# Kernel tuning notes

Measured on AMD Instinct MI355X. Metric: run time of the kernel, lower is better.

Reference implementation:

```python
import jax, jax.numpy as jnp
import numpy as np

SLOPE = 25.0   # fast_sigmoid surrogate slope (affects backward only)
THRESH = 1.0   # snntorch Leaky default threshold

@jax.custom_vjp
def spike(x):
    # Heaviside forward, fast-sigmoid surrogate backward
    return (x > 0).astype(x.dtype)

def _spike_fwd(x):
    return spike(x), x

def _spike_bwd(x, g):
    return (g / (SLOPE * jnp.abs(x) + 1.0) ** 2,)

spike.defvjp(_spike_fwd, _spike_bwd)


def setup_inputs() -> dict:
    key = jax.random.key(0)
    ks = jax.random.split(key, 16)
    B, T, F = 512, 1024, 64
    SNN, H, HOR = 128, 128, 24
    s = 0.05
    inp = {
        "x": jax.random.normal(ks[0], (B, T, F), jnp.float32),
        "proj_w": jax.random.normal(ks[1], (SNN, F), jnp.float32) * s,
        "proj_b": jnp.zeros((SNN,), jnp.float32),
        "beta1": jnp.full((SNN,), 0.9, jnp.float32),
        "beta2": jnp.full((SNN,), 0.9, jnp.float32),
        "gru_w_ih": jax.random.normal(ks[2], (3 * H, F + SNN), jnp.float32) * s,
        "gru_w_hh": jax.random.normal(ks[3], (3 * H, H), jnp.float32) * s,
        "gru_b_ih": jnp.zeros((3 * H,), jnp.float32),
        "gru_b_hh": jnp.zeros((3 * H,), jnp.float32),
        "attn_w1": jax.random.normal(ks[4], (H // 2, H), jnp.float32) * s,
        "attn_b1": jnp.zeros((H // 2,), jnp.float32),
        "attn_w2": jax.random.normal(ks[5], (1, H // 2), jnp.float32) * s,
        "attn_b2": jnp.zeros((1,), jnp.float32),
        "head_w": jax.random.normal(ks[6], (HOR, H), jnp.float32) * s,
        "head_b": jnp.zeros((HOR,), jnp.float32),
    }
    return inp


def reference(x, proj_w, proj_b, beta1, beta2,
              gru_w_ih, gru_w_hh, gru_b_ih, gru_b_hh,
              attn_w1, attn_b1, attn_w2, attn_b2, head_w, head_b):
    b1 = jnp.clip(beta1, 0.0, 0.99)
    b2 = jnp.clip(beta2, 0.0, 0.99)

    delta = x[:, 1:, :] - x[:, :-1, :]   # (B, T-1, F)
    raw = x[:, 1:, :]
    h_s = delta @ proj_w.T + proj_b      # (B, T-1, SNN)

    B = x.shape[0]
    SNN = proj_w.shape[0]

    # snntorch Leaky (subtract reset, reset from previous step's spike):
    # mem_t = beta*mem_{t-1} + in_t - spk_{t-1}*thr ; spk_t = H(mem_t - thr)
    def snn_step(carry, inp_t):
        m1, s1, m2, s2 = carry
        m1 = b1 * m1 + inp_t - s1 * THRESH
        s1n = spike(m1 - THRESH)
        m2 = b2 * m2 + s1n - s2 * THRESH
        s2n = spike(m2 - THRESH)
        return (m1, s1n, m2, s2n), m2

    z = jnp.zeros((B, SNN), x.dtype)
    _, mem_rec = jax.lax.scan(snn_step, (z, z, z, z), jnp.swapaxes(h_s, 0, 1))
    h_snn = jnp.swapaxes(mem_rec, 0, 1)             # (B, T-1, SNN)

    h_comb = jnp.concatenate([raw, h_snn], axis=-1)  # (B, T-1, F+SNN)

    # GRU (PyTorch gate layout: r, z, n)
    H = gru_w_hh.shape[1]
    x_proj = h_comb @ gru_w_ih.T + gru_b_ih          # (B, T-1, 3H)

    def gru_step(h, xp):
        gh = h @ gru_w_hh.T + gru_b_hh
        xr, xz, xn = jnp.split(xp, 3, axis=-1)
        hr, hz, hn = jnp.split(gh, 3, axis=-1)
        r = jax.nn.sigmoid(xr + hr)
        zg = jax.nn.sigmoid(xz + hz)
        n = jnp.tanh(xn + r * hn)
        h_new = (1.0 - zg) * n + zg * h
        return h_new, h_new

    h0 = jnp.zeros((B, H), x.dtype)
    _, gru_seq = jax.lax.scan(gru_step, h0, jnp.swapaxes(x_proj, 0, 1))
    gru_out = jnp.swapaxes(gru_seq, 0, 1)            # (B, T-1, H)

    # Temporal attention over time (dim=1)
    scores = jax.nn.relu(gru_out @ attn_w1.T + attn_b1) @ attn_w2.T + attn_b2  # (B, T-1, 1)
    w = jax.nn.softmax(scores, axis=1)
    h_ann = (w * gru_out).sum(axis=1)                # (B, H)

    return h_ann @ head_w.T + head_b                 # (B, horizon)
```

## Files before the change

kernel.cpp:

```cpp
#include <hip/hip_runtime.h>

typedef unsigned short u16;
typedef __attribute__((ext_vector_type(8))) short short8;
typedef __attribute__((ext_vector_type(4))) float f32x4;

__device__ __forceinline__ u16 f2bf(float f) {
  union { float f; unsigned u; } v; v.f = f;
  unsigned r = v.u + 0x7fffu + ((v.u >> 16) & 1u);
  return (u16)(r >> 16);
}
__device__ __forceinline__ u16 truncbf(float f) {
  union { float f; unsigned u; } v; v.f = f;
  return (u16)(v.u >> 16);
}
__device__ __forceinline__ float bf2f(u16 h) {
  union { unsigned u; float f; } v; v.u = ((unsigned)h) << 16;
  return v.f;
}
__device__ __forceinline__ void gll16(const void* g, void* l) {
  __builtin_amdgcn_global_load_lds((const __attribute__((address_space(1))) unsigned*)g,
                                   (__attribute__((address_space(3))) unsigned*)l, 16, 0, 0);
}
__device__ __forceinline__ void bar_lds() {
  asm volatile("s_waitcnt lgkmcnt(0)" ::: "memory");
  __builtin_amdgcn_s_barrier();
  asm volatile("" ::: "memory");
}

#define BATCH 512
#define TS 1023
#define NF 64
#define NS 128
#define NH 128
#define NG 384
#define NC 192
#define TCH 341

__global__ void k_prep(const float* __restrict__ wih, const float* __restrict__ w1,
                       u16* __restrict__ wihb, u16* __restrict__ w1b) {
  int i = blockIdx.x * 256 + threadIdx.x;
  if (i < NG * NC) wihb[i] = f2bf(wih[i]);
  if (i < 64 * NH) w1b[i] = f2bf(w1[i]);
}

__global__ __launch_bounds__(256, 2) void k_front(const float* __restrict__ x,
                                                  const float* __restrict__ pw,
                                                  const float* __restrict__ pb,
                                                  const float* __restrict__ beta1,
                                                  const float* __restrict__ beta2,
                                                  u16* __restrict__ hcomb) {
  __shared__ float hst[64 * 138];
  const int tid = threadIdx.x, lane = tid & 63, w = tid >> 6;
  const int m16 = lane & 15, quad = lane >> 4;
  const int b = blockIdx.x;
  const float* xb = x + (long)b * 65536;

  const int tm = (w >> 1) * 32, nn = (w & 1) * 64;

  short8 bh[2][4], bl[2][4];
  #pragma unroll
  for (int kc = 0; kc < 2; ++kc)
    #pragma unroll
    for (int ni = 0; ni < 4; ++ni) {
      const float* src = pw + (nn + ni * 16 + m16) * 64 + kc * 32 + quad * 8;
      f32x4 v0 = *(const f32x4*)src;
      f32x4 v1 = *(const f32x4*)(src + 4);
      #pragma unroll
      for (int jj = 0; jj < 8; ++jj) {
        float v = (jj < 4) ? v0[jj & 3] : v1[jj & 3];
        u16 hh = truncbf(v);
        bh[kc][ni][jj] = (short)hh;
        bl[kc][ni][jj] = (short)f2bf(v - bf2f(hh));
      }
    }

  float b1v = 0.f, b2v = 0.f, m1 = 0.f, s1 = 0.f, m2 = 0.f, s2 = 0.f;
  if (tid < 128) {
    b1v = fminf(fmaxf(beta1[tid], 0.f), 0.99f);
    b2v = fminf(fmaxf(beta2[tid], 0.f), 0.99f);
  }
  float pbv[4];
  #pragma unroll
  for (int ni = 0; ni < 4; ++ni) pbv[ni] = pb[nn + ni * 16 + m16];

  for (int tile = 0; tile < 16; ++tile) {
    const int t0 = tile * 64;
    const int tl = (TS - t0 < 64) ? (TS - t0) : 64;

    f32x4 acc[2][4] = {};
    #pragma unroll
    for (int kc = 0; kc < 2; ++kc) {
      short8 ah[2], al[2];
      #pragma unroll
      for (int mi = 0; mi < 2; ++mi) {
        int row = tm + mi * 16 + m16;
        int tA = t0 + row; if (tA > 1022) tA = 1022;
        const float* p0 = xb + (long)tA * 64 + kc * 32 + quad * 8;
        f32x4 lo0 = *(const f32x4*)p0;
        f32x4 lo1 = *(const f32x4*)(p0 + 4);
        f32x4 hi0 = *(const f32x4*)(p0 + 64);
        f32x4 hi1 = *(const f32x4*)(p0 + 68);
        float d[8];
        #pragma unroll
        for (int jj = 0; jj < 4; ++jj) { d[jj] = hi0[jj] - lo0[jj]; d[4 + jj] = hi1[jj] - lo1[jj]; }
        #pragma unroll
        for (int jj = 0; jj < 8; ++jj) {
          u16 hh = truncbf(d[jj]);
          ah[mi][jj] = (short)hh;
          al[mi][jj] = (short)f2bf(d[jj] - bf2f(hh));
        }
      }
      #pragma unroll
      for (int mi = 0; mi < 2; ++mi)
        #pragma unroll
        for (int ni = 0; ni < 4; ++ni) {
          acc[mi][ni] = __builtin_amdgcn_mfma_f32_16x16x32_bf16(ah[mi], bh[kc][ni], acc[mi][ni], 0, 0, 0);
          acc[mi][ni] = __builtin_amdgcn_mfma_f32_16x16x32_bf16(ah[mi], bl[kc][ni], acc[mi][ni], 0, 0, 0);
          acc[mi][ni] = __builtin_amdgcn_mfma_f32_16x16x32_bf16(al[mi], bh[kc][ni], acc[mi][ni], 0, 0, 0);
        }
    }
    #pragma unroll
    for (int mi = 0; mi < 2; ++mi)
      #pragma unroll
      for (int ni = 0; ni < 4; ++ni)
        #pragma unroll
        for (int rr = 0; rr < 4; ++rr)
          hst[(tm + mi * 16 + quad * 4 + rr) * 138 + nn + ni * 16 + m16] = acc[mi][ni][rr] + pbv[ni];
    bar_lds();
    if (tid < 128) {
      const int n = tid;
      u16* dst = hcomb + ((long)t0 * 512 + b) * NC + 64 + n;
      for (int tt = 0; tt < tl; tt += 8) {
        float v[8];
        #pragma unroll
        for (int jj = 0; jj < 8; ++jj) {
          int t = tt + jj; if (t > 63) t = 63;
          v[jj] = hst[t * 138 + n];
        }
        #pragma unroll
        for (int jj = 0; jj < 8; ++jj) {
          int t = tt + jj;
          if (t < tl) {
            m1 = b1v * m1 + v[jj] - s1;
            s1 = (m1 > 1.0f) ? 1.0f : 0.0f;
            m2 = b2v * m2 + s1 - s2;
            s2 = (m2 > 1.0f) ? 1.0f : 0.0f;
            dst[(long)t * (512 * NC)] = f2bf(m2);
          }
        }
      }
    } else {
      const int f = tid & 63, half = (tid >> 6) & 1;
      for (int r = half; r < tl; r += 2)
        hcomb[((long)(t0 + r) * 512 + b) * NC + f] = f2bf(xb[(long)(t0 + r + 1) * 64 + f]);
    }
    bar_lds();
  }
}

__global__ __launch_bounds__(256) void k_xproj(const u16* __restrict__ hc, const u16* __restrict__ wih,
                                               const float* __restrict__ bih, u16* __restrict__ xp) {
  __shared__ alignas(16) u16 As[4096], Bs[4096];
  const int tid = threadIdx.x, lane = tid & 63, w = tid >> 6;
  const int m16 = lane & 15, quad = lane >> 4;
  const long row0 = (long)blockIdx.x * 128;
  const int n0 = blockIdx.y * 128;
  const int wm = (w >> 1) * 64, wn = (w & 1) * 64;
  f32x4 acc[4][4] = {};
  const char* gA = (const char*)hc + (row0 + (lane >> 2)) * (NC * 2) + (lane & 3) * 16;
  const char* gB = (const char*)wih + (long)(n0 + (lane >> 2)) * (NC * 2) + (lane & 3) * 16;
  for (int kc = 0; kc < 6; ++kc) {
    #pragma unroll
    for (int i = 0; i < 2; ++i) {
      int q = i * 4 + w;
      gll16(gA + (long)q * 16 * (NC * 2) + kc * 64, (char*)As + q * 1024);
      gll16(gB + (long)q * 16 * (NC * 2) + kc * 64, (char*)Bs + q * 1024);
    }
    __syncthreads();
    short8 af[4], bfr[4];
    #pragma unroll
    for (int mi = 0; mi < 4; ++mi) af[mi] = *(const short8*)((const char*)As + (wm + mi * 16 + m16) * 64 + quad * 16);
    #pragma unroll
    for (int ni = 0; ni < 4; ++ni) bfr[ni] = *(const short8*)((const char*)Bs + (wn + ni * 16 + m16) * 64 + quad * 16);
    #pragma unroll
    for (int mi = 0; mi < 4; ++mi)
      #pragma unroll
      for (int ni = 0; ni < 4; ++ni)
        acc[mi][ni] = __builtin_amdgcn_mfma_f32_16x16x32_bf16(af[mi], bfr[ni], acc[mi][ni], 0, 0, 0);
    __syncthreads();
  }
  #pragma unroll
  for (int ni = 0; ni < 4; ++ni) {
    int n = n0 + wn + ni * 16 + m16;
    float bias = bih[n];
    #pragma unroll
    for (int mi = 0; mi < 4; ++mi) {
      long r = row0 + wm + mi * 16 + quad * 4;
      #pragma unroll
      for (int rr = 0; rr < 4; ++rr)
        xp[(r + rr) * NG + n] = f2bf(acc[mi][ni][rr] + bias);
    }
  }
}

__device__ __forceinline__ void score_body(long row0, const u16* __restrict__ gbf, const u16* __restrict__ w1,
                                           const float* __restrict__ b1, const float* __restrict__ w2,
                                           const float* __restrict__ b2, float* __restrict__ scores,
                                           u16* Gs, u16* Ws) {
  const int tid = threadIdx.x, lane = tid & 63, w = tid >> 6;
  const int m16 = lane & 15, quad = lane >> 4;
  f32x4 acc[2][4] = {};
  const char* gG = (const char*)gbf + (row0 + (lane >> 2)) * (NH * 2) + (lane & 3) * 16;
  const char* gW = (const char*)w1 + (long)(w * 16 + (lane >> 2)) * (NH * 2) + (lane & 3) * 16;
  for (int kc = 0; kc < 4; ++kc) {
    #pragma unroll
    for (int i = 0; i < 2; ++i) {
      int q = i * 4 + w;
      gll16(gG + (long)q * 16 * (NH * 2) + kc * 64, (char*)Gs + q * 1024);
    }
    gll16(gW + kc * 64, (char*)Ws + w * 1024);
    __syncthreads();
    short8 af[2], bfr[4];
    #pragma unroll
    for (int mi = 0; mi < 2; ++mi) af[mi] = *(const short8*)((const char*)Gs + (w * 32 + mi * 16 + m16) * 64 + quad * 16);
    #pragma unroll
    for (int ni = 0; ni < 4; ++ni) bfr[ni] = *(const short8*)((const char*)Ws + (ni * 16 + m16) * 64 + quad * 16);
    #pragma unroll
    for (int mi = 0; mi < 2; ++mi)
      #pragma unroll
      for (int ni = 0; ni < 4; ++ni)
        acc[mi][ni] = __builtin_amdgcn_mfma_f32_16x16x32_bf16(af[mi], bfr[ni], acc[mi][ni], 0, 0, 0);
    __syncthreads();
  }
  float b2v = b2[0];
  float w2v[4], b1v[4];
  #pragma unroll
  for (int ni = 0; ni < 4; ++ni) { w2v[ni] = w2[ni * 16 + m16]; b1v[ni] = b1[ni * 16 + m16]; }
  #pragma unroll
  for (int mi = 0; mi < 2; ++mi) {
    #pragma unroll
    for (int rr = 0; rr < 4; ++rr) {
      float v = 0.f;
      #pragma unroll
      for (int ni = 0; ni < 4; ++ni) {
        float hv = acc[mi][ni][rr] + b1v[ni];
        hv = hv > 0.f ? hv : 0.f;
        v = fmaf(hv, w2v[ni], v);
      }
      v += __shfl_xor(v, 1, 64); v += __shfl_xor(v, 2, 64);
      v += __shfl_xor(v, 4, 64); v += __shfl_xor(v, 8, 64);
      if (m16 == 0) scores[row0 + w * 32 + mi * 16 + quad * 4 + rr] = v + b2v;
    }
  }
}

__global__ __launch_bounds__(256) void k_score(const u16* __restrict__ gbf, const u16* __restrict__ w1,
                                               const float* __restrict__ b1, const float* __restrict__ w2,
                                               const float* __restrict__ b2, float* __restrict__ scores,
                                               long row_base) {
  __shared__ alignas(16) u16 Gs[4096], Ws[2048];
  score_body(row_base + (long)blockIdx.x * 128, gbf, w1, b1, w2, b2, scores, Gs, Ws);
}

__global__ __launch_bounds__(256, 2) void k_gru(const u16* __restrict__ xp, const float* __restrict__ whh,
                                                const float* __restrict__ bhh, u16* __restrict__ gout,
                                                float* __restrict__ h_state, int first,
                                                const u16* __restrict__ gbf, const u16* __restrict__ w1,
                                                const float* __restrict__ b1, const float* __restrict__ w2,
                                                const float* __restrict__ b2, float* __restrict__ scores,
                                                long score_base) {
  __shared__ alignas(16) u16 frag[2 * 2048];
  __shared__ alignas(16) u16 Gs[4096], Ws[2048];
  if (blockIdx.x >= 256) {
    score_body(score_base + (long)(blockIdx.x - 256) * 128, gbf, w1, b1, w2, b2, scores, Gs, Ws);
    return;
  }
  const int tid = threadIdx.x, lane = tid & 63, w = tid >> 6;
  const int m16 = lane & 15, quad = lane >> 4;
  const long bg0 = (long)blockIdx.x * 2;
  {
    short8 z8 = {};
    *(short8*)((char*)frag + tid * 16) = z8;
    *(short8*)((char*)frag + 4096 + tid * 16) = z8;
  }
  short8 wf[6][4];
  #pragma unroll
  for (int g = 0; g < 3; ++g)
    #pragma unroll
    for (int hh = 0; hh < 2; ++hh)
      #pragma unroll
      for (int c = 0; c < 4; ++c) {
        const float* src = whh + (long)(g * 128 + 32 * w + hh * 16 + m16) * NH + c * 32 + quad * 8;
        short8 v;
        #pragma unroll
        for (int jj = 0; jj < 8; ++jj) v[jj] = (short)f2bf(src[jj]);
        wf[g * 2 + hh][c] = v;
      }
  const int bq = quad & 1, hq = quad >> 1;
  const int j = 32 * w + hq * 16 + m16;
  const long brow = bg0 + bq;
  const float br_ = bhh[j], bz_ = bhh[128 + j], bn_ = bhh[256 + j];
  float h = first ? 0.f : h_state[brow * NH + j];
  const int fragoff = w * 1024 + 64 * bq + 256 * (hq * 2 + (m16 >> 3)) + 2 * (m16 & 7);
  __syncthreads();
  {
    u16 hb0 = f2bf(h);
    *(u16*)((char*)frag + fragoff) = hb0;
    *(u16*)((char*)frag + fragoff + 128) = hb0;
  }
  const u16* xbase = xp + brow * NG + j;
  u16 pr[8], pz[8], pn[8], sbuf[8];
  #pragma unroll
  for (int u = 0; u < 8; ++u) {
    const u16* xr = xbase + (long)u * (512 * NG);
    pr[u] = xr[0]; pz[u] = xr[128]; pn[u] = xr[256];
  }
  __syncthreads();

#define GRU_STEP(T, U)                                                                     \
  {                                                                                        \
    const int cur = ((T) & 1) * 4096, nxt = 4096 - cur;                                    \
    short8 af[4];                                                                          \
    _Pragma("unroll")                                                                      \
    for (int c = 0; c < 4; ++c)                                                            \
      af[c] = *(const short8*)((const char*)frag + cur + c * 1024 + lane * 16);            \
    f32x4 zero = {0.f, 0.f, 0.f, 0.f};                                                     \
    f32x4 accA[6], accB[6];                                                                \
    _Pragma("unroll")                                                                      \
    for (int nt = 0; nt < 6; ++nt) {                                                       \
      accA[nt] = __builtin_amdgcn_mfma_f32_16x16x32_bf16(af[0], wf[nt][0], zero, 0, 0, 0); \
      accB[nt] = __builtin_amdgcn_mfma_f32_16x16x32_bf16(af[2], wf[nt][2], zero, 0, 0, 0); \
    }                                                                                      \
    _Pragma("unroll")                                                                      \
    for (int nt = 0; nt < 6; ++nt) {                                                       \
      accA[nt] = __builtin_amdgcn_mfma_f32_16x16x32_bf16(af[1], wf[nt][1], accA[nt], 0, 0, 0); \
      accB[nt] = __builtin_amdgcn_mfma_f32_16x16x32_bf16(af[3], wf[nt][3], accB[nt], 0, 0, 0); \
    }                                                                                      \
    float ghr = (hq ? (accA[1][0] + accB[1][0]) : (accA[0][0] + accB[0][0])) + br_;        \
    float ghz = (hq ? (accA[3][0] + accB[3][0]) : (accA[2][0] + accB[2][0])) + bz_;        \
    float ghn = (hq ? (accA[5][0] + accB[5][0]) : (accA[4][0] + accB[4][0])) + bn_;        \
    float xrv = bf2f(pr[U]), xzv = bf2f(pz[U]), xnv = bf2f(pn[U]);                         \
    float rg = 1.f / (1.f + __expf(-(xrv + ghr)));                                         \
    float zg = 1.f / (1.f + __expf(-(xzv + ghz)));                                         \
    float niv = xnv + rg * ghn;                                                            \
    float ng = 1.f - 2.f / (1.f + __expf(2.f * niv));                                      \
    h = (1.f - zg) * ng + zg * h;                                                          \
    u16 hb = f2bf(h);                                                                      \
    sbuf[U] = hb;                                                                          \
    *(u16*)((char*)frag + nxt + fragoff) = hb;                                             \
    *(u16*)((char*)frag + nxt + fragoff + 128) = hb;                                       \
    __syncthreads();                                                                       \
  }

  for (int t8 = 0; t8 < 336; t8 += 8) {
    if (t8 > 0) {
      #pragma unroll
      for (int u = 0; u < 8; ++u)
        gout[((long)(t8 - 8 + u) * 512 + brow) * NH + j] = sbuf[u];
    }
    u16 npr[8], npz[8], npn[8];
    #pragma unroll
    for (int u = 0; u < 8; ++u) {
      long tp = t8 + 8 + u; if (tp > TCH - 1) tp = TCH - 1;
      const u16* xr = xbase + tp * (512 * NG);
      npr[u] = xr[0]; npz[u] = xr[128]; npn[u] = xr[256];
    }
    GRU_STEP(t8 + 0, 0) GRU_STEP(t8 + 1, 1) GRU_STEP(t8 + 2, 2) GRU_STEP(t8 + 3, 3)
    GRU_STEP(t8 + 4, 4) GRU_STEP(t8 + 5, 5) GRU_STEP(t8 + 6, 6) GRU_STEP(t8 + 7, 7)
    #pragma unroll
    for (int u = 0; u < 8; ++u) { pr[u] = npr[u]; pz[u] = npz[u]; pn[u] = npn[u]; }
  }
  #pragma unroll
  for (int u = 0; u < 8; ++u)
    gout[((long)(328 + u) * 512 + brow) * NH + j] = sbuf[u];
  #pragma unroll
  for (int u = 0; u < 5; ++u) {
    GRU_STEP(336 + u, u)
    gout[((long)(336 + u) * 512 + brow) * NH + j] = sbuf[u];
  }
#undef GRU_STEP
  h_state[brow * NH + j] = h;
}

__global__ __launch_bounds__(256) void k_attn(const float* __restrict__ scores, const u16* __restrict__ gout,
                                              const float* __restrict__ headw, const float* __restrict__ headb,
                                              float* __restrict__ out) {
  __shared__ float sc[TS];
  __shared__ float red[8];
  __shared__ float part[8][132];
  __shared__ float hann[128];
  const int tid = threadIdx.x, lane = tid & 63, w = tid >> 6;
  const long b = blockIdx.x;
  const float* srow = scores + b;
  float s0[4];
  #pragma unroll
  for (int i = 0; i < 4; ++i) {
    int t = tid + i * 256;
    s0[i] = (t < TS) ? srow[(long)t * 512] : -1e30f;
  }
  float mx = fmaxf(fmaxf(s0[0], s0[1]), fmaxf(s0[2], s0[3]));
  #pragma unroll
  for (int off = 32; off > 0; off >>= 1) mx = fmaxf(mx, __shfl_xor(mx, off, 64));
  if (lane == 0) red[w] = mx;
  __syncthreads();
  mx = fmaxf(fmaxf(red[0], red[1]), fmaxf(red[2], red[3]));
  float sum = 0.f;
  #pragma unroll
  for (int i = 0; i < 4; ++i) {
    int t = tid + i * 256;
    if (t < TS) { float e = __expf(s0[i] - mx); sc[t] = e; sum += e; }
  }
  #pragma unroll
  for (int off = 32; off > 0; off >>= 1) sum += __shfl_xor(sum, off, 64);
  if (lane == 0) red[4 + w] = sum;
  __syncthreads();
  float inv = 1.f / (red[4] + red[5] + red[6] + red[7]);
  const int jg = tid & 31, sl = tid >> 5;
  float acc[4] = {0.f, 0.f, 0.f, 0.f};
  const u16* gbase = gout + b * NH + jg * 4;
  for (int t = sl; t < TS; t += 8) {
    float wt = sc[t];
    ushort4 g4 = *(const ushort4*)(gbase + (long)t * (512 * NH));
    acc[0] = fmaf(wt, bf2f(g4.x), acc[0]);
    acc[1] = fmaf(wt, bf2f(g4.y), acc[1]);
    acc[2] = fmaf(wt, bf2f(g4.z), acc[2]);
    acc[3] = fmaf(wt, bf2f(g4.w), acc[3]);
  }
  #pragma unroll
  for (int i = 0; i < 4; ++i) part[sl][jg * 4 + i] = acc[i];
  __syncthreads();
  if (tid < 128) {
    float v = 0.f;
    #pragma unroll
    for (int s = 0; s < 8; ++s) v += part[s][tid];
    hann[tid] = v * inv;
  }
  __syncthreads();
  if (tid < 24) {
    float a = headb[tid];
    const float* hwr = headw + tid * 128;
    for (int k = 0; k < 128; k += 4) {
      float4 h4 = *(const float4*)&hann[k];
      float4 w4 = *(const float4*)&hwr[k];
      a = fmaf(h4.x, w4.x, a); a = fmaf(h4.y, w4.y, a);
      a = fmaf(h4.z, w4.z, a); a = fmaf(h4.w, w4.w, a);
    }
    out[b * 24 + tid] = a;
  }
}

extern "C" void kernel_launch(void* const* d_in, const int* in_sizes, int n_in,
                              void* d_out, int out_size, void* d_ws, size_t ws_size,
                              hipStream_t stream) {
  const float* x      = (const float*)d_in[0];
  const float* proj_w = (const float*)d_in[1];
  const float* proj_b = (const float*)d_in[2];
  const float* beta1  = (const float*)d_in[3];
  const float* beta2  = (const float*)d_in[4];
  const float* gwih   = (const float*)d_in[5];
  const float* gwhh   = (const float*)d_in[6];
  const float* gbih   = (const float*)d_in[7];
  const float* gbhh   = (const float*)d_in[8];
  const float* aw1    = (const float*)d_in[9];
  const float* ab1    = (const float*)d_in[10];
  const float* aw2    = (const float*)d_in[11];
  const float* ab2    = (const float*)d_in[12];
  const float* hw     = (const float*)d_in[13];
  const float* hb     = (const float*)d_in[14];
  float* out = (float*)d_out;
  char* ws = (char*)d_ws;

  u16*   hcomb  = (u16*)(ws);
  u16*   xpbuf  = (u16*)(ws + 201129984L);
  u16*   gru    = (u16*)(ws + 335216640L);
  float* scores = (float*)(ws + 469303296L);
  u16*   wihb   = (u16*)(ws + 471398400L);
  u16*   w1b    = (u16*)(ws + 471545856L);
  float* hstate = (float*)(ws + 471562240L);

  k_prep<<<288, 256, 0, stream>>>(gwih, aw1, wihb, w1b);
  k_front<<<512, 256, 0, stream>>>(x, proj_w, proj_b, beta1, beta2, hcomb);
  for (int c = 0; c < 3; ++c) {
    long rowbase = (long)c * TCH * 512;
    k_xproj<<<dim3(1364, 3), 256, 0, stream>>>(hcomb + rowbase * NC, wihb, gbih, xpbuf);
    int grid = (c == 0) ? 256 : 256 + 1364;
    long score_base = (long)(c - 1) * TCH * 512;
    k_gru<<<grid, 256, 0, stream>>>(xpbuf, gwhh, gbhh, gru + rowbase * NH, hstate, c == 0 ? 1 : 0,
                                    gru, w1b, ab1, aw2, ab2, scores, score_base);
  }
  k_score<<<1364, 256, 0, stream>>>(gru, w1b, ab1, aw2, ab2, scores, 2L * TCH * 512);
  k_attn<<<512, 256, 0, stream>>>(scores, gru, hw, hb, out);
}
```

Baseline: 1.069 ms.

## Double-buffer xproj into GRU launches with smaller time chunks

Splits the time sequence into eight chunks of 128 steps instead of three of 341. The input projection for the next chunk now runs as extra blocks inside the GRU launch, writing into a second ping-pong buffer, alongside the score blocks for the previous chunk. This takes the standalone xproj launches off the serial GRU critical path so they overlap the latency-bound recurrence. The cost is more launches and tail handling for variable step counts, and the extra blocks compete with the GRU blocks for CUs.

```diff
diff --git a/kernel.cpp b/kernel.cpp
--- a/kernel.cpp
+++ b/kernel.cpp
@@ -34,7 +34,7 @@
 #define NH 128
 #define NG 384
 #define NC 192
-#define TCH 341
+#define CH 128
 
 __global__ void k_prep(const float* __restrict__ wih, const float* __restrict__ w1,
                        u16* __restrict__ wihb, u16* __restrict__ w1b) {
@@ -158,13 +158,11 @@
   }
 }
 
-__global__ __launch_bounds__(256) void k_xproj(const u16* __restrict__ hc, const u16* __restrict__ wih,
-                                               const float* __restrict__ bih, u16* __restrict__ xp) {
-  __shared__ alignas(16) u16 As[4096], Bs[4096];
+__device__ __forceinline__ void xproj_body(long row0, int n0, const u16* __restrict__ hc,
+                                           const u16* __restrict__ wih, const float* __restrict__ bih,
+                                           u16* __restrict__ xp, u16* As, u16* Bs) {
   const int tid = threadIdx.x, lane = tid & 63, w = tid >> 6;
   const int m16 = lane & 15, quad = lane >> 4;
-  const long row0 = (long)blockIdx.x * 128;
-  const int n0 = blockIdx.y * 128;
   const int wm = (w >> 1) * 64, wn = (w & 1) * 64;
   f32x4 acc[4][4] = {};
   const char* gA = (const char*)hc + (row0 + (lane >> 2)) * (NC * 2) + (lane & 3) * 16;
@@ -201,6 +199,12 @@
         xp[(r + rr) * NG + n] = f2bf(acc[mi][ni][rr] + bias);
     }
   }
+}
+
+__global__ __launch_bounds__(256) void k_xproj(const u16* __restrict__ hc, const u16* __restrict__ wih,
+                                               const float* __restrict__ bih, u16* __restrict__ xp) {
+  __shared__ alignas(16) u16 As[4096], Bs[4096];
+  xproj_body((long)blockIdx.x * 128, blockIdx.y * 128, hc, wih, bih, xp, As, Bs);
 }
 
 __device__ __forceinline__ void score_body(long row0, const u16* __restrict__ gbf, const u16* __restrict__ w1,
@@ -264,15 +268,22 @@
 
 __global__ __launch_bounds__(256, 2) void k_gru(const u16* __restrict__ xp, const float* __restrict__ whh,
                                                 const float* __restrict__ bhh, u16* __restrict__ gout,
-                                                float* __restrict__ h_state, int first,
+                                                float* __restrict__ h_state, int first, int nsteps,
+                                                const u16* __restrict__ hcN, const u16* __restrict__ wihb,
+                                                const float* __restrict__ bih, u16* __restrict__ xpN,
+                                                int nxr, int nxp,
                                                 const u16* __restrict__ gbf, const u16* __restrict__ w1,
                                                 const float* __restrict__ b1, const float* __restrict__ w2,
                                                 const float* __restrict__ b2, float* __restrict__ scores,
                                                 long score_base) {
   __shared__ alignas(16) u16 frag[2 * 2048];
-  __shared__ alignas(16) u16 Gs[4096], Ws[2048];
+  __shared__ alignas(16) u16 smem[8192];
   if (blockIdx.x >= 256) {
-    score_body(score_base + (long)(blockIdx.x - 256) * 128, gbf, w1, b1, w2, b2, scores, Gs, Ws);
+    int ebid = blockIdx.x - 256;
+    if (ebid < nxp)
+      xproj_body((long)(ebid % nxr) * 128, (ebid / nxr) * 128, hcN, wihb, bih, xpN, smem, smem + 4096);
+    else
+      score_body(score_base + (long)(ebid - nxp) * 128, gbf, w1, b1, w2, b2, scores, smem, smem + 4096);
     return;
   }
   const int tid = threadIdx.x, lane = tid & 63, w = tid >> 6;
@@ -352,7 +363,8 @@
     __syncthreads();                                                                       \
   }
 
-  for (int t8 = 0; t8 < 336; t8 += 8) {
+  const int N8 = nsteps & ~7;
+  for (int t8 = 0; t8 < N8; t8 += 8) {
     if (t8 > 0) {
       #pragma unroll
       for (int u = 0; u < 8; ++u)
@@ -361,7 +373,7 @@
     u16 npr[8], npz[8], npn[8];
     #pragma unroll
     for (int u = 0; u < 8; ++u) {
-      long tp = t8 + 8 + u; if (tp > TCH - 1) tp = TCH - 1;
+      long tp = t8 + 8 + u; if (tp > nsteps - 1) tp = nsteps - 1;
       const u16* xr = xbase + tp * (512 * NG);
       npr[u] = xr[0]; npz[u] = xr[128]; npn[u] = xr[256];
     }
@@ -372,11 +384,14 @@
   }
   #pragma unroll
   for (int u = 0; u < 8; ++u)
-    gout[((long)(328 + u) * 512 + brow) * NH + j] = sbuf[u];
-  #pragma unroll
-  for (int u = 0; u < 5; ++u) {
-    GRU_STEP(336 + u, u)
-    gout[((long)(336 + u) * 512 + brow) * NH + j] = sbuf[u];
+    gout[((long)(N8 - 8 + u) * 512 + brow) * NH + j] = sbuf[u];
+  const int tail = nsteps & 7;
+  #pragma unroll
+  for (int u = 0; u < 7; ++u) {
+    if (u < tail) {
+      GRU_STEP(N8 + u, u)
+      gout[((long)(N8 + u) * 512 + brow) * NH + j] = sbuf[u];
+    }
   }
 #undef GRU_STEP
   h_state[brow * NH + j] = h;
@@ -478,16 +493,25 @@
   u16*   w1b    = (u16*)(ws + 471545856L);
   float* hstate = (float*)(ws + 471562240L);
 
+  u16* slot[2] = {xpbuf, xpbuf + 25165824L};
+
   k_prep<<<288, 256, 0, stream>>>(gwih, aw1, wihb, w1b);
   k_front<<<512, 256, 0, stream>>>(x, proj_w, proj_b, beta1, beta2, hcomb);
-  for (int c = 0; c < 3; ++c) {
-    long rowbase = (long)c * TCH * 512;
-    k_xproj<<<dim3(1364, 3), 256, 0, stream>>>(hcomb + rowbase * NC, wihb, gbih, xpbuf);
-    int grid = (c == 0) ? 256 : 256 + 1364;
-    long score_base = (long)(c - 1) * TCH * 512;
-    k_gru<<<grid, 256, 0, stream>>>(xpbuf, gwhh, gbhh, gru + rowbase * NH, hstate, c == 0 ? 1 : 0,
-                                    gru, w1b, ab1, aw2, ab2, scores, score_base);
-  }
-  k_score<<<1364, 256, 0, stream>>>(gru, w1b, ab1, aw2, ab2, scores, 2L * TCH * 512);
+  k_xproj<<<dim3(512, 3), 256, 0, stream>>>(hcomb, wihb, gbih, slot[0]);
+  for (int c = 0; c < 8; ++c) {
+    int len = (c == 7) ? 127 : 128;
+    long start = (long)c * CH;
+    int lenN = (c + 1 == 7) ? 127 : 128;
+    int nxr = (c < 7) ? (lenN * 512 / 128) : 0;
+    int nxp = nxr * 3;
+    int nsc = (c >= 1) ? 512 : 0;
+    const u16* hcN = hcomb + (start + len) * 512L * NC;
+    long score_base = (c >= 1) ? ((long)(c - 1) * CH * 512) : 0;
+    k_gru<<<256 + nxp + nsc, 256, 0, stream>>>(
+        slot[c & 1], gwhh, gbhh, gru + start * 512L * NH, hstate, c == 0 ? 1 : 0, len,
+        hcN, wihb, gbih, slot[(c + 1) & 1], nxr, nxp,
+        gru, w1b, ab1, aw2, ab2, scores, score_base);
+  }
+  k_score<<<508, 256, 0, stream>>>(gru, w1b, ab1, aw2, ab2, scores, 896L * 512);
   k_attn<<<512, 256, 0, stream>>>(scores, gru, hw, hb, out);
 }
```

Measured after the change: 964.8 us. 1.11x faster.
